# Optimization experiments

Measured on AMD Instinct MI355X. Metric: run time of the kernel, lower is better.

The kernel has to match this reference:

```python
import jax, jax.numpy as jnp
import numpy as np
from jax import lax

TEMP = 0.1
EPS_LOG = 1e-6
RMS_EPS = 1e-6
K_NEIGHBORS = 8


def setup_inputs() -> dict:
    key = jax.random.key(0)
    ks = jax.random.split(key, 8)
    B, T, D = 2, 2048, 1024
    N, DK, DM = 32768, 256, 256
    return {
        "x": jax.random.normal(ks[0], (B, T, D), dtype=jnp.float32),
        "keys": jax.random.normal(ks[1], (N, DK), dtype=jnp.float32),
        "vals": jax.random.normal(ks[2], (N, DM), dtype=jnp.float32),
        "W_in": jax.random.normal(ks[3], (DK, D), dtype=jnp.float32) / np.sqrt(D),
        "b_in": jnp.zeros((DK,), dtype=jnp.float32),
        "W_out": jax.random.normal(ks[4], (D, K_NEIGHBORS * DM), dtype=jnp.float32) / np.sqrt(K_NEIGHBORS * DM),
        "b_out": jnp.zeros((D,), dtype=jnp.float32),
        "rms_w": jnp.ones((D,), dtype=jnp.float32),
    }


def _memory_forward(x, keys, vals, W_in, b_in, W_out, b_out, rms_w):
    B, T, D = x.shape
    N, DM = vals.shape
    # proj_in: [B,T,D] -> [B,T,DK]
    q = jnp.einsum("btd,kd->btk", x, W_in) + b_in
    # squared euclidean distances to memory keys: [B,T,N]
    q2 = jnp.sum(q * q, axis=-1, keepdims=True)          # [B,T,1]
    k2 = jnp.sum(keys * keys, axis=-1)                   # [N]
    qk = jnp.einsum("btc,nc->btn", q, keys)              # [B,T,N]
    logits = -(q2 - 2.0 * qk + k2) / TEMP                # [B,T,N]

    # N3Net-style continuous k-NN: k rounds of softmax selection
    def step(lg, _):
        w = jax.nn.softmax(lg, axis=-1)                  # [B,T,N]
        out = jnp.einsum("btn,nf->btf", w, vals)         # [B,T,DM]
        lg = lg + jnp.log1p(-w + EPS_LOG)
        return lg, out

    _, outs = lax.scan(step, logits, None, length=K_NEIGHBORS)  # [K,B,T,DM]
    nearest = jnp.moveaxis(outs, 0, 2).reshape(B, T, K_NEIGHBORS * DM)

    out = jnp.einsum("btf,df->btd", nearest, W_out) + b_out
    # RMSNorm
    var = jnp.mean(out.astype(jnp.float32) ** 2, axis=-1, keepdims=True)
    out = out * lax.rsqrt(var + RMS_EPS)
    return rms_w * out


def reference(x, keys, vals, W_in, b_in, W_out, b_out, rms_w):
    return _memory_forward(x, keys, vals, W_in, b_in, W_out, b_out, rms_w)
```

## Files before the change

kernel.cpp:

```cpp
#include <hip/hip_runtime.h>
#include <hip/hip_bf16.h>

#define ROWS  4096
#define DDIM  1024
#define DKDIM 256
#define NKEYS 32768
#define DMDIM 256
#define KN    8
#define FDIM  2048
#define CAPS  1536
#define SLOT  184
#define SURV  128
#define SURV2 96
#define MARGIN   16.0f
#define REFILT_M 12.25f
#define EXACT_M  109.0f

typedef float  f32x4  __attribute__((ext_vector_type(4)));
typedef __bf16 bf16x8 __attribute__((ext_vector_type(8)));

static __device__ __forceinline__ unsigned enc_f32(float f) {
  unsigned u = __float_as_uint(f);
  return u ^ ((unsigned)((int)u >> 31) | 0x80000000u);
}
static __device__ __forceinline__ float dec_f32(unsigned u) {
  unsigned b = (u & 0x80000000u) ? (u ^ 0x80000000u) : ~u;
  return __uint_as_float(b);
}
static __device__ __forceinline__ unsigned short f2bf(float f) {
  unsigned u = __float_as_uint(f);
  u += 0x7FFFu + ((u >> 16) & 1u);
  return (unsigned short)(u >> 16);
}
static __device__ __forceinline__ unsigned pack_cand(float s, int n) {
  float q = (s + 1024.f) * 64.f;
  int u = (int)q;
  u = u < 0 ? 0 : (u > 131071 ? 131071 : u);
  return ((unsigned)u << 15) | (unsigned)n;
}
static __device__ __forceinline__ float cand_score(unsigned p) {
  return (float)(p >> 15) * (1.f / 64.f) - 1024.f;
}
static __device__ __forceinline__ void gld16(const void* g, void* l) {
  __builtin_amdgcn_global_load_lds((const __attribute__((address_space(1))) void*)g,
                                   (__attribute__((address_space(3))) void*)l, 16, 0, 0);
}

__global__ __launch_bounds__(256) void prep_all(const float* __restrict__ keys,
                                                const float* __restrict__ Wout,
                                                unsigned short* __restrict__ kbf,
                                                float* __restrict__ k2,
                                                unsigned short* __restrict__ wbf,
                                                unsigned* __restrict__ rowmax) {
  const int b = blockIdx.x, t = threadIdx.x;
  if (b < 8192) {
    const int row = b * 4 + (t >> 6);
    const int ln  = t & 63;
    const float4 v = *(const float4*)(keys + (size_t)row * DKDIM + ln * 4);
    ushort4 o;
    o.x = f2bf(v.x); o.y = f2bf(v.y); o.z = f2bf(v.z); o.w = f2bf(v.w);
    *(ushort4*)(kbf + (size_t)row * DKDIM + ln * 4) = o;
    float ss = v.x*v.x + v.y*v.y + v.z*v.z + v.w*v.w;
    for (int off = 32; off; off >>= 1) ss += __shfl_down(ss, off);
    if (ln == 0) k2[row] = ss;
  } else if (b < 10240) {
    const int i = (b - 8192) * 256 + t;
    const float4 v = *(const float4*)(Wout + (size_t)i * 4);
    ushort4 o;
    o.x = f2bf(v.x); o.y = f2bf(v.y); o.z = f2bf(v.z); o.w = f2bf(v.w);
    *(ushort4*)(wbf + (size_t)i * 4) = o;
  } else {
    rowmax[(b - 10240) * 256 + t] = 0u;
  }
}

__global__ __launch_bounds__(256) void qproj(const float* __restrict__ x,
                                             const float* __restrict__ Win,
                                             const float* __restrict__ bin,
                                             float* __restrict__ qf,
                                             unsigned short* __restrict__ qbf) {
  __shared__ __align__(16) float As[64][68];
  __shared__ __align__(16) float Bs[64][68];
  const int bm = blockIdx.x, bn = blockIdx.y;
  const int t  = threadIdx.x;
  const int tx = t & 15, ty = t >> 4;
  float acc[4][4] = {};
  for (int ks = 0; ks < 16; ++ks) {
    __syncthreads();
    for (int l = t; l < 1024; l += 256) {
      const int row = l >> 4, kc = l & 15;
      *(float4*)(&As[row][kc * 4]) =
          *(const float4*)(x + (size_t)(bm * 64 + row) * DDIM + ks * 64 + kc * 4);
      *(float4*)(&Bs[row][kc * 4]) =
          *(const float4*)(Win + (size_t)(bn * 64 + row) * DDIM + ks * 64 + kc * 4);
    }
    __syncthreads();
    for (int kk = 0; kk < 64; kk += 4) {
      float4 av[4], bv[4];
#pragma unroll
      for (int i = 0; i < 4; ++i) av[i] = *(const float4*)(&As[ty * 4 + i][kk]);
#pragma unroll
      for (int j = 0; j < 4; ++j) bv[j] = *(const float4*)(&Bs[tx * 4 + j][kk]);
#pragma unroll
      for (int i = 0; i < 4; ++i)
#pragma unroll
        for (int j = 0; j < 4; ++j)
          acc[i][j] += av[i].x * bv[j].x + av[i].y * bv[j].y +
                       av[i].z * bv[j].z + av[i].w * bv[j].w;
    }
  }
#pragma unroll
  for (int i = 0; i < 4; ++i)
#pragma unroll
    for (int j = 0; j < 4; ++j) {
      const int m = bm * 64 + ty * 4 + i, n = bn * 64 + tx * 4 + j;
      const float q = acc[i][j] + bin[n];
      qf[(size_t)m * DKDIM + n] = q;
      qbf[(size_t)m * DKDIM + n] = f2bf(q);
    }
}

template <int KD>
static __device__ __forceinline__ void gemm_tile(const unsigned short* __restrict__ A,
                                                 const unsigned short* __restrict__ B,
                                                 int bm, int bn,
                                                 unsigned short* As, unsigned short* Bs,
                                                 f32x4 acc[4][4]) {
  const int tid  = threadIdx.x;
  const int lane = tid & 63, wave = tid >> 6;
  const int quad = lane >> 4, l15 = lane & 15;
  const int wr = (wave >> 1) * 64, wc = (wave & 1) * 64;
  const int srow = tid >> 2, skc = tid & 3;
  const unsigned short* gA = A + (size_t)(bm * 128 + srow) * KD + skc * 8;
  const unsigned short* gB = B + (size_t)(bn * 128 + srow) * KD + skc * 8;
  for (int ks = 0; ks < KD / 32; ++ks) {
    __syncthreads();
    gld16(gA + ks * 32,                     As + tid * 8);
    gld16(gA + (size_t)64 * KD + ks * 32,   As + 2048 + tid * 8);
    gld16(gB + ks * 32,                     Bs + tid * 8);
    gld16(gB + (size_t)64 * KD + ks * 32,   Bs + 2048 + tid * 8);
    __syncthreads();
    bf16x8 af[4], bfr[4];
#pragma unroll
    for (int i = 0; i < 4; ++i)
      af[i] = *(const bf16x8*)(As + (wr + i * 16 + l15) * 32 + quad * 8);
#pragma unroll
    for (int j = 0; j < 4; ++j)
      bfr[j] = *(const bf16x8*)(Bs + (wc + j * 16 + l15) * 32 + quad * 8);
#pragma unroll
    for (int i = 0; i < 4; ++i)
#pragma unroll
      for (int j = 0; j < 4; ++j)
        acc[i][j] = __builtin_amdgcn_mfma_f32_16x16x32_bf16(af[i], bfr[j], acc[i][j], 0, 0, 0);
  }
}

__global__ __launch_bounds__(512) void score_select(const unsigned short* __restrict__ qbf,
                                                    const unsigned short* __restrict__ kbf,
                                                    const float* __restrict__ k2,
                                                    unsigned* __restrict__ rowmax,
                                                    int* __restrict__ cnt,
                                                    unsigned* __restrict__ cand) {
  __shared__ __align__(16) unsigned short Al[8 * 4096];
  __shared__ __align__(16) unsigned short Bl[3 * 8192];
  __shared__ __align__(16) float k2s[4096];
  __shared__ float wm[128][4];
  __shared__ float thr[128];
  __shared__ float lmax[128];
  __shared__ int   pcnt[128];
  const int cg = blockIdx.x, bm = blockIdx.y;
  const int t = threadIdx.x;
  const int lane = t & 63, wave = t >> 6;
  const int quad = lane >> 4, l15 = lane & 15;
  const int wr = (wave >> 2) * 64, wc = (wave & 3) * 64;
  const unsigned short* gA = qbf + (size_t)(bm * 128 + (t >> 2)) * DKDIM + (t & 3) * 8;
  const unsigned short* gB = kbf + ((size_t)cg * 4096 + (t >> 2)) * DKDIM + (t & 3) * 8;

  if (t < 128) { lmax[t] = -3.4e38f; pcnt[t] = 0; }

#pragma unroll
  for (int ks = 0; ks < 8; ++ks)
    gld16(gA + ks * 32, Al + ks * 4096 + t * 8);
  {
    const float* gk = k2 + (size_t)cg * 4096;
#pragma unroll
    for (int i = 0; i < 2; ++i)
      gld16(gk + i * 2048 + t * 4, (char*)k2s + i * 8192 + t * 16);
  }
#pragma unroll
  for (int c0 = 0; c0 < 2; ++c0) {
    gld16(gB + c0 * 32, Bl + c0 * 8192 + t * 8);
    gld16(gB + (size_t)128 * DKDIM + c0 * 32, Bl + c0 * 8192 + 4096 + t * 8);
  }

  f32x4 acc[4][4] = {};
  int bcur = 0;
  for (int tile = 0; tile < 16; ++tile) {
    unsigned rstale = 0u;
    if (t < 128) rstale = rowmax[bm * 128 + t];
#pragma unroll
    for (int ks = 0; ks < 8; ++ks) {
      if (tile == 15 && ks == 7)
        asm volatile("s_waitcnt vmcnt(0)" ::: "memory");
      else if (ks == 0)
        asm volatile("s_waitcnt vmcnt(3)" ::: "memory");
      else
        asm volatile("s_waitcnt vmcnt(2)" ::: "memory");
      __builtin_amdgcn_s_barrier();
      asm volatile("" ::: "memory");
      {
        const int cn = tile * 8 + ks + 2;
        if (cn < 128) {
          const int bst = bcur == 0 ? 2 : bcur - 1;
          const unsigned short* src = gB + (size_t)(cn >> 3) * 256 * DKDIM + (cn & 7) * 32;
          gld16(src, Bl + bst * 8192 + t * 8);
          gld16(src + (size_t)128 * DKDIM, Bl + bst * 8192 + 4096 + t * 8);
        }
      }
      const unsigned short* Ap = Al + ks * 4096;
      const unsigned short* Bp = Bl + bcur * 8192;
      bf16x8 af[4], bv[4];
#pragma unroll
      for (int i = 0; i < 4; ++i)
        af[i] = *(const bf16x8*)(Ap + (wr + i * 16 + l15) * 32 + quad * 8);
#pragma unroll
      for (int j = 0; j < 4; ++j)
        bv[j] = *(const bf16x8*)(Bp + (wc + j * 16 + l15) * 32 + quad * 8);
#pragma unroll
      for (int i = 0; i < 4; ++i)
#pragma unroll
        for (int j = 0; j < 4; ++j)
          acc[i][j] = __builtin_amdgcn_mfma_f32_16x16x32_bf16(af[i], bv[j], acc[i][j], 0, 0, 0);
      bcur = bcur == 2 ? 0 : bcur + 1;
    }
    float k2v[4];
#pragma unroll
    for (int j = 0; j < 4; ++j) k2v[j] = k2s[tile * 256 + wc + j * 16 + l15];
#pragma unroll
    for (int i = 0; i < 4; ++i)
#pragma unroll
      for (int r = 0; r < 4; ++r) {
        float v = -3.4e38f;
#pragma unroll
        for (int j = 0; j < 4; ++j) v = fmaxf(v, 2.f * acc[i][j][r] - k2v[j]);
        for (int m = 8; m; m >>= 1) v = fmaxf(v, __shfl_xor(v, m));
        if (l15 == 0) wm[wr + i * 16 + quad * 4 + r][wave & 3] = v;
      }
    asm volatile("s_waitcnt lgkmcnt(0)" ::: "memory");
    __builtin_amdgcn_s_barrier();
    asm volatile("" ::: "memory");
    if (t < 128) {
      const float tmax = fmaxf(fmaxf(wm[t][0], wm[t][1]), fmaxf(wm[t][2], wm[t][3]));
      const float run = fmaxf(lmax[t], tmax);
      lmax[t] = run;
      (void)atomicMax(&rowmax[bm * 128 + t], enc_f32(run));
      thr[t] = fmaxf(run, dec_f32(rstale)) - MARGIN;
    }
    asm volatile("s_waitcnt lgkmcnt(0)" ::: "memory");
    __builtin_amdgcn_s_barrier();
    asm volatile("" ::: "memory");
#pragma unroll
    for (int i = 0; i < 4; ++i)
#pragma unroll
      for (int r = 0; r < 4; ++r) {
        const int rl = wr + i * 16 + quad * 4 + r;
        const float th = thr[rl];
#pragma unroll
        for (int j = 0; j < 4; ++j) {
          const float s = 2.f * acc[i][j][r] - k2v[j];
          if (s >= th) {
            const int n = cg * 4096 + tile * 256 + wc + j * 16 + l15;
            const int pos = atomicAdd(&pcnt[rl], 1);
            if (pos < SLOT)
              cand[((size_t)(bm * 128 + rl) * 8 + cg) * SLOT + pos] = pack_cand(s, n);
          }
        }
      }
#pragma unroll
    for (int i = 0; i < 4; ++i)
#pragma unroll
      for (int j = 0; j < 4; ++j)
#pragma unroll
        for (int r2 = 0; r2 < 4; ++r2) acc[i][j][r2] = 0.f;
  }
  __syncthreads();
  if (t < 128) cnt[(size_t)(bm * 128 + t) * 8 + cg] = min(pcnt[t], SLOT);
}

__global__ __launch_bounds__(256) void knn_rounds(const float* __restrict__ qf,
                                                  const float* __restrict__ keys,
                                                  const float* __restrict__ k2,
                                                  const float* __restrict__ vals,
                                                  const int* __restrict__ cnt,
                                                  const unsigned* __restrict__ cand,
                                                  unsigned short* __restrict__ nearest) {
  __shared__ __align__(16) float qs[DKDIM];
  __shared__ unsigned cl[CAPS];
  __shared__ float red[256];
  __shared__ int   sidx[SURV];
  __shared__ float Ls[SURV];
  __shared__ int   sidx2[SURV2];
  __shared__ float L2v[SURV2];
  __shared__ float cs[SURV2];
  __shared__ float Ws[SURV2 * KN];
  __shared__ int n1, n2;
  const int row = blockIdx.x, t = threadIdx.x;
  qs[t] = qf[(size_t)row * DKDIM + t];
  if (t == 0) { n1 = 0; n2 = 0; }
  float m = -3.4e38f;
  int C = 0;
  for (int s8 = 0; s8 < 8; ++s8) {
    const int Cs = min(cnt[(size_t)row * 8 + s8], SLOT);
    const unsigned* cp = cand + ((size_t)row * 8 + s8) * SLOT;
    for (int i = t; i < Cs; i += 256) {
      const unsigned p = cp[i];
      cl[C + i] = p;
      m = fmaxf(m, cand_score(p));
    }
    C += Cs;
  }
  red[t] = m;
  __syncthreads();
  for (int s = 128; s; s >>= 1) {
    if (t < s) red[t] = fmaxf(red[t], red[t + s]);
    __syncthreads();
  }
  const float th1 = red[0] - REFILT_M;
  for (int i = t; i < C; i += 256) {
    if (cand_score(cl[i]) >= th1) {
      const int p = atomicAdd(&n1, 1);
      if (p < SURV) sidx[p] = (int)(cl[i] & 32767u);
    }
  }
  if (t < SURV2) cs[t] = 0.f;
  __syncthreads();
  const int S1 = min(n1, SURV);
  const int wv = t >> 6, ln = t & 63;
  for (int i = wv; i < S1; i += 4) {
    const int n = sidx[i];
    const float4 kv = *(const float4*)(keys + (size_t)n * DKDIM + ln * 4);
    const float4 qv = *(const float4*)(qs + ln * 4);
    float d = kv.x * qv.x + kv.y * qv.y + kv.z * qv.z + kv.w * qv.w;
    for (int o = 32; o; o >>= 1) d += __shfl_down(d, o);
    if (ln == 0) Ls[i] = (2.f * d - k2[n]) / 0.1f;
  }
  __syncthreads();
  red[t] = (t < S1) ? Ls[t] : -3.4e38f;
  __syncthreads();
  for (int s = 128; s; s >>= 1) {
    if (t < s) red[t] = fmaxf(red[t], red[t + s]);
    __syncthreads();
  }
  const float Lmax = red[0];
  if (t < S1 && Ls[t] >= Lmax - EXACT_M) {
    const int p = atomicAdd(&n2, 1);
    if (p < SURV2) { sidx2[p] = sidx[t]; L2v[p] = Ls[t]; }
  }
  __syncthreads();
  const int S2 = min(n2, SURV2);
  if (t < 64) {
    for (int j = 0; j < KN; ++j) {
      float lm = -3.4e38f;
      for (int i = t; i < S2; i += 64) lm = fmaxf(lm, L2v[i] + cs[i]);
      for (int o = 32; o; o >>= 1) lm = fmaxf(lm, __shfl_xor(lm, o));
      float zs = 0.f;
      for (int i = t; i < S2; i += 64) {
        const float e = expf(L2v[i] + cs[i] - lm);
        Ws[i * KN + j] = e; zs += e;
      }
      for (int o = 32; o; o >>= 1) zs += __shfl_xor(zs, o);
      const float Zi = 1.f / zs;
      for (int i = t; i < S2; i += 64) {
        const float w = Ws[i * KN + j] * Zi;
        Ws[i * KN + j] = w;
        cs[i] += log1pf(1e-6f - w);
      }
    }
  }
  __syncthreads();
  float acc[KN] = {};
  for (int i = 0; i < S2; ++i) {
    const float v = vals[(size_t)sidx2[i] * DMDIM + t];
#pragma unroll
    for (int j = 0; j < KN; ++j) acc[j] += Ws[i * KN + j] * v;
  }
#pragma unroll
  for (int j = 0; j < KN; ++j)
    nearest[(size_t)row * FDIM + j * DMDIM + t] = f2bf(acc[j]);
}

__global__ __launch_bounds__(256) void out_gemm(const unsigned short* __restrict__ nbf,
                                                const unsigned short* __restrict__ wbf,
                                                const float* __restrict__ bout,
                                                float* __restrict__ out) {
  __shared__ __align__(16) unsigned short As[4096];
  __shared__ __align__(16) unsigned short Bs[4096];
  f32x4 acc[4][4] = {};
  gemm_tile<FDIM>(nbf, wbf, blockIdx.x, blockIdx.y, As, Bs, acc);
  const int lane = threadIdx.x & 63, wave = threadIdx.x >> 6;
  const int quad = lane >> 4, l15 = lane & 15;
  const int wr = (wave >> 1) * 64, wc = (wave & 1) * 64;
#pragma unroll
  for (int i = 0; i < 4; ++i)
#pragma unroll
    for (int r = 0; r < 4; ++r) {
      const int gm = blockIdx.x * 128 + wr + i * 16 + quad * 4 + r;
#pragma unroll
      for (int j = 0; j < 4; ++j) {
        const int n = blockIdx.y * 128 + wc + j * 16 + l15;
        out[(size_t)gm * DDIM + n] = acc[i][j][r] + bout[n];
      }
    }
}

__global__ __launch_bounds__(256) void rmsnorm(float* __restrict__ out,
                                               const float* __restrict__ rmsw) {
  __shared__ float red[256];
  const int row = blockIdx.x, t = threadIdx.x;
  const float4 v = *(const float4*)(out + (size_t)row * DDIM + t * 4);
  red[t] = v.x * v.x + v.y * v.y + v.z * v.z + v.w * v.w;
  __syncthreads();
  for (int s = 128; s; s >>= 1) {
    if (t < s) red[t] += red[t + s];
    __syncthreads();
  }
  const float scale = rsqrtf(red[0] / (float)DDIM + 1e-6f);
  const float4 w = *(const float4*)(rmsw + t * 4);
  float4 o;
  o.x = v.x * scale * w.x; o.y = v.y * scale * w.y;
  o.z = v.z * scale * w.z; o.w = v.w * scale * w.w;
  *(float4*)(out + (size_t)row * DDIM + t * 4) = o;
}

extern "C" void kernel_launch(void* const* d_in, const int* in_sizes, int n_in,
                              void* d_out, int out_size, void* d_ws, size_t ws_size,
                              hipStream_t stream) {
  const float* x    = (const float*)d_in[0];
  const float* keys = (const float*)d_in[1];
  const float* vals = (const float*)d_in[2];
  const float* Win  = (const float*)d_in[3];
  const float* bin  = (const float*)d_in[4];
  const float* Wout = (const float*)d_in[5];
  const float* bout = (const float*)d_in[6];
  const float* rmsw = (const float*)d_in[7];
  float* out = (float*)d_out;
  char* ws = (char*)d_ws;

  float*          q_f32   = (float*)(ws);
  unsigned short* q_bf    = (unsigned short*)(ws + 4194304);
  unsigned short* k_bf    = (unsigned short*)(ws + 6291456);
  unsigned short* nearest = (unsigned short*)(ws + 6291456);
  float*          k2      = (float*)(ws + 23068672);
  unsigned*       rowmax  = (unsigned*)(ws + 23199744);
  int*            cnt     = (int*)(ws + 23216128);
  unsigned*       cand    = (unsigned*)(ws + 23347200);
  unsigned short* w_bf    = (unsigned short*)(ws + 47464448);

  prep_all<<<10256, 256, 0, stream>>>(keys, Wout, k_bf, k2, w_bf, rowmax);
  qproj<<<dim3(ROWS / 64, DKDIM / 64), 256, 0, stream>>>(x, Win, bin, q_f32, q_bf);
  score_select<<<dim3(8, 32), 512, 0, stream>>>(q_bf, k_bf, k2, rowmax, cnt, cand);
  knn_rounds<<<ROWS, 256, 0, stream>>>(q_f32, keys, k2, vals, cnt, cand, nearest);
  out_gemm<<<dim3(ROWS / 128, DDIM / 128), 256, 0, stream>>>(nearest, w_bf, bout, out);
  rmsnorm<<<ROWS, 256, 0, stream>>>(out, rmsw);
}
```

Baseline: 465.1 us.

## Restructure score_select GEMM pipeline with four LDS buffers and conflict-free layout

Replaces the triple-buffered B tile ring with four named LDS buffers and a macro-unrolled eight-phase loop. Each phase loads its fragments, then issues the prefetch, waits and synchronises, with MFMA priority raised via s_setprio. The A and B tiles are rearranged into a quad-major layout so fragment reads are contiguous. The aim is better overlap of global loads with MFMA and fewer LDS bank conflicts. The cost is more LDS use and two barriers per phase.

```diff
diff --git a/kernel.cpp b/kernel.cpp
--- a/kernel.cpp
+++ b/kernel.cpp
@@ -162,7 +162,10 @@
                                                     int* __restrict__ cnt,
                                                     unsigned* __restrict__ cand) {
   __shared__ __align__(16) unsigned short Al[8 * 4096];
-  __shared__ __align__(16) unsigned short Bl[3 * 8192];
+  __shared__ __align__(16) unsigned short Bq0[8192];
+  __shared__ __align__(16) unsigned short Bq1[8192];
+  __shared__ __align__(16) unsigned short Bq2[8192];
+  __shared__ __align__(16) unsigned short Bq3[8192];
   __shared__ __align__(16) float k2s[4096];
   __shared__ float wm[128][4];
   __shared__ float thr[128];
@@ -173,66 +176,78 @@
   const int lane = t & 63, wave = t >> 6;
   const int quad = lane >> 4, l15 = lane & 15;
   const int wr = (wave >> 2) * 64, wc = (wave & 3) * 64;
-  const unsigned short* gA = qbf + (size_t)(bm * 128 + (t >> 2)) * DKDIM + (t & 3) * 8;
-  const unsigned short* gB = kbf + ((size_t)cg * 4096 + (t >> 2)) * DKDIM + (t & 3) * 8;
 
   if (t < 128) { lmax[t] = -3.4e38f; pcnt[t] = 0; }
 
-#pragma unroll
-  for (int ks = 0; ks < 8; ++ks)
-    gld16(gA + ks * 32, Al + ks * 4096 + t * 8);
   {
+    const unsigned short* gA = qbf + (size_t)(bm * 128 + (t & 127)) * DKDIM + (t >> 7) * 8;
+#pragma unroll
+    for (int ks = 0; ks < 8; ++ks)
+      gld16(gA + ks * 32, Al + ks * 4096 + t * 8);
     const float* gk = k2 + (size_t)cg * 4096;
 #pragma unroll
     for (int i = 0; i < 2; ++i)
       gld16(gk + i * 2048 + t * 4, (char*)k2s + i * 8192 + t * 16);
-  }
-#pragma unroll
-  for (int c0 = 0; c0 < 2; ++c0) {
-    gld16(gB + c0 * 32, Bl + c0 * 8192 + t * 8);
-    gld16(gB + (size_t)128 * DKDIM + c0 * 32, Bl + c0 * 8192 + 4096 + t * 8);
+    const unsigned short* sb0 = kbf + ((size_t)cg * 4096 + (t & 255)) * DKDIM + (t >> 8) * 8;
+    gld16(sb0,      Bq0 + t * 8);
+    gld16(sb0 + 16, Bq0 + 4096 + t * 8);
+    gld16(sb0 + 32, Bq1 + t * 8);
+    gld16(sb0 + 48, Bq1 + 4096 + t * 8);
+  }
+  asm volatile("s_waitcnt vmcnt(0)" ::: "memory");
+  __builtin_amdgcn_s_barrier();
+  asm volatile("" ::: "memory");
+
+#define PREFETCH(CN, BUF)                                                                  \
+  {                                                                                        \
+    const unsigned short* sb = kbf + ((size_t)cg * 4096 + (size_t)((CN) >> 3) * 256 +      \
+                                      (t & 255)) * DKDIM + ((CN) & 7) * 32 + (t >> 8) * 8; \
+    gld16(sb,      (BUF) + t * 8);                                                         \
+    gld16(sb + 16, (BUF) + 4096 + t * 8);                                                  \
+  }
+
+#define PHASE(KS, CUR, NXT)                                                                \
+  {                                                                                        \
+    bf16x8 af[4], bv[4];                                                                   \
+    {                                                                                      \
+      const unsigned short* Ap = Al + (KS) * 4096 + quad * 1024;                           \
+      const unsigned short* Bp = (CUR) + quad * 2048;                                      \
+      _Pragma("unroll") for (int i = 0; i < 4; ++i)                                        \
+        af[i] = *(const bf16x8*)(Ap + (wr + i * 16 + l15) * 8);                            \
+      _Pragma("unroll") for (int j = 0; j < 4; ++j)                                        \
+        bv[j] = *(const bf16x8*)(Bp + (wc + j * 16 + l15) * 8);                            \
+    }                                                                                      \
+    if ((KS) == 0 && tile > 0) {                                                           \
+      asm volatile("s_waitcnt vmcnt(0)" ::: "memory");   \
+      PREFETCH(tile * 8 + (KS) + 2, NXT);               \
+    } else if (tile * 8 + (KS) + 2 < 128) {                                                \
+      PREFETCH(tile * 8 + (KS) + 2, NXT);                                                  \
+      asm volatile("s_waitcnt vmcnt(2)" ::: "memory");     \
+    } else {                                                                               \
+      asm volatile("s_waitcnt vmcnt(0)" ::: "memory");                  \
+    }                                                                                      \
+    __builtin_amdgcn_s_barrier();                                   \
+    asm volatile("" ::: "memory");                                                         \
+    __builtin_amdgcn_s_setprio(1);                                                         \
+    _Pragma("unroll") for (int i = 0; i < 4; ++i)                                          \
+      _Pragma("unroll") for (int j = 0; j < 4; ++j)                                        \
+        acc[i][j] = __builtin_amdgcn_mfma_f32_16x16x32_bf16(af[i], bv[j], acc[i][j], 0, 0, 0); \
+    __builtin_amdgcn_s_setprio(0);                                                         \
+    __builtin_amdgcn_s_barrier();                                                          \
+    asm volatile("" ::: "memory");                                                         \
   }
 
   f32x4 acc[4][4] = {};
-  int bcur = 0;
   for (int tile = 0; tile < 16; ++tile) {
-    unsigned rstale = 0u;
-    if (t < 128) rstale = rowmax[bm * 128 + t];
-#pragma unroll
-    for (int ks = 0; ks < 8; ++ks) {
-      if (tile == 15 && ks == 7)
-        asm volatile("s_waitcnt vmcnt(0)" ::: "memory");
-      else if (ks == 0)
-        asm volatile("s_waitcnt vmcnt(3)" ::: "memory");
-      else
-        asm volatile("s_waitcnt vmcnt(2)" ::: "memory");
-      __builtin_amdgcn_s_barrier();
-      asm volatile("" ::: "memory");
-      {
-        const int cn = tile * 8 + ks + 2;
-        if (cn < 128) {
-          const int bst = bcur == 0 ? 2 : bcur - 1;
-          const unsigned short* src = gB + (size_t)(cn >> 3) * 256 * DKDIM + (cn & 7) * 32;
-          gld16(src, Bl + bst * 8192 + t * 8);
-          gld16(src + (size_t)128 * DKDIM, Bl + bst * 8192 + 4096 + t * 8);
-        }
-      }
-      const unsigned short* Ap = Al + ks * 4096;
-      const unsigned short* Bp = Bl + bcur * 8192;
-      bf16x8 af[4], bv[4];
-#pragma unroll
-      for (int i = 0; i < 4; ++i)
-        af[i] = *(const bf16x8*)(Ap + (wr + i * 16 + l15) * 32 + quad * 8);
-#pragma unroll
-      for (int j = 0; j < 4; ++j)
-        bv[j] = *(const bf16x8*)(Bp + (wc + j * 16 + l15) * 32 + quad * 8);
-#pragma unroll
-      for (int i = 0; i < 4; ++i)
-#pragma unroll
-        for (int j = 0; j < 4; ++j)
-          acc[i][j] = __builtin_amdgcn_mfma_f32_16x16x32_bf16(af[i], bv[j], acc[i][j], 0, 0, 0);
-      bcur = bcur == 2 ? 0 : bcur + 1;
-    }
+    const unsigned rstale = rowmax[bm * 128 + (t & 127)];
+    PHASE(0, Bq0, Bq2)
+    PHASE(1, Bq1, Bq3)
+    PHASE(2, Bq2, Bq0)
+    PHASE(3, Bq3, Bq1)
+    PHASE(4, Bq0, Bq2)
+    PHASE(5, Bq1, Bq3)
+    PHASE(6, Bq2, Bq0)
+    PHASE(7, Bq3, Bq1)
     float k2v[4];
 #pragma unroll
     for (int j = 0; j < 4; ++j) k2v[j] = k2s[tile * 256 + wc + j * 16 + l15];
@@ -283,6 +298,8 @@
 #pragma unroll
         for (int r2 = 0; r2 < 4; ++r2) acc[i][j][r2] = 0.f;
   }
+#undef PHASE
+#undef PREFETCH
   __syncthreads();
   if (t < 128) cnt[(size_t)(bm * 128 + t) * 8 + cg] = min(pcnt[t], SLOT);
 }
```

Measured after the change: 479.7 us. +3.1%, slower.
